# Optimization experiments

Hardware: AMD Instinct MI355X
Metric: run time of the kernel (lower is better)

Reference implementation:

```python
import jax, jax.numpy as jnp
import numpy as np

EPS = 1e-5  # torch LayerNorm default


def _layer_norm(x, g, b):
    mu = jnp.mean(x, axis=-1, keepdims=True)
    var = jnp.mean(jnp.square(x - mu), axis=-1, keepdims=True)
    return (x - mu) * jax.lax.rsqrt(var + EPS) * g + b


def setup_inputs() -> dict:
    key = jax.random.key(0)
    ks = jax.random.split(key, 8)
    B, S, D = 4, 2048, 1024
    s = 1.0 / np.sqrt(D)
    return {
        "q": jax.random.normal(ks[0], (B, S, D), jnp.float32),
        "k": jax.random.normal(ks[1], (B, S, D), jnp.float32),
        "v": jax.random.normal(ks[2], (B, S, D), jnp.float32),
        "mask": jnp.ones((B, 1, S), jnp.int32),
        "Wq": jax.random.normal(ks[3], (D, D), jnp.float32) * s,
        "Wk": jax.random.normal(ks[4], (D, D), jnp.float32) * s,
        "Wv": jax.random.normal(ks[5], (D, D), jnp.float32) * s,
        "Wo": jax.random.normal(ks[6], (D, D), jnp.float32) * s,
        "ln_q_g": jnp.ones((D,), jnp.float32),
        "ln_q_b": jnp.zeros((D,), jnp.float32),
        "ln_k_g": jnp.ones((D,), jnp.float32),
        "ln_k_b": jnp.zeros((D,), jnp.float32),
        "ln_v_g": jnp.ones((D,), jnp.float32),
        "ln_v_b": jnp.zeros((D,), jnp.float32),
    }


def reference(q, k, v, mask, Wq, Wk, Wv, Wo,
              ln_q_g, ln_q_b, ln_k_g, ln_k_b, ln_v_g, ln_v_b):
    B, Lq, D = q.shape
    H = 16
    dk = D // H
    residual = q
    # pre-LN + bias-free projections
    qh = (_layer_norm(q, ln_q_g, ln_q_b) @ Wq).reshape(B, Lq, H, dk).transpose(0, 2, 1, 3)
    kh = (_layer_norm(k, ln_k_g, ln_k_b) @ Wk).reshape(B, -1, H, dk).transpose(0, 2, 1, 3)
    vh = (_layer_norm(v, ln_v_g, ln_v_b) @ Wv).reshape(B, -1, H, dk).transpose(0, 2, 1, 3)
    # scaled scores [B,H,Lq,Lk]
    scores = jnp.einsum('bhqd,bhkd->bhqk', qh, kh) / jnp.sqrt(jnp.float32(dk))
    pad = (mask == 0)[:, None, :, :]  # [B,1,*,Lk], True where masked
    scores = jnp.where(pad, -jnp.inf, scores)
    attn = jax.nn.softmax(scores, axis=-1)
    attn = jnp.where(pad, 0.0, attn)
    out = jnp.einsum('bhqk,bhkd->bhqd', attn, vh)
    out = out.transpose(0, 2, 1, 3).reshape(B, Lq, D)
    return out @ Wo + residual
```

## Files before the change

### kernel.cpp

```cpp
#include <hip/hip_runtime.h>
#include <stdint.h>

typedef __attribute__((ext_vector_type(8))) short short8;
typedef __attribute__((ext_vector_type(4))) float f32x4;
typedef __attribute__((ext_vector_type(4))) unsigned short us4;

#define B_ 4
#define S_ 2048
#define D_ 1024
#define H_ 16
#define DK_ 64

__device__ __forceinline__ unsigned short f2bf(float f) {
  union { float f; unsigned int u; } c; c.f = f;
  unsigned int r = (c.u + 0x7fffu + ((c.u >> 16) & 1u)) >> 16;
  return (unsigned short)r;
}

__device__ __forceinline__ unsigned int cvt_pk_bf16(float lo, float hi) {
  unsigned int r;
  asm("v_cvt_pk_bf16_f32 %0, %1, %2" : "=v"(r) : "v"(lo), "v"(hi));
  return r;
}

__device__ __forceinline__ float exp2_fast(float x) {
#if __has_builtin(__builtin_amdgcn_exp2f)
  return __builtin_amdgcn_exp2f(x);
#else
  float r; asm("v_exp_f32 %0, %1" : "=v"(r) : "v"(x)); return r;
#endif
}

__device__ __forceinline__ void glds16(const void* g, void* l) {
  __builtin_amdgcn_global_load_lds(
      (__attribute__((address_space(1))) void*)(uintptr_t)g,
      (__attribute__((address_space(3))) void*)l, 16, 0, 0);
}

__device__ __forceinline__ f32x4 mfma_bf16(short8 a, short8 b, f32x4 c) {
  return __builtin_amdgcn_mfma_f32_16x16x32_bf16(a, b, c, 0, 0, 0);
}

__global__ __launch_bounds__(256) void ln_bf16_3(const float* __restrict__ x0,
                                                 const float* __restrict__ x1,
                                                 const float* __restrict__ x2,
                                                 const float* __restrict__ g0,
                                                 const float* __restrict__ g1,
                                                 const float* __restrict__ g2,
                                                 const float* __restrict__ b0,
                                                 const float* __restrict__ b1,
                                                 const float* __restrict__ b2,
                                                 unsigned short* __restrict__ y0,
                                                 unsigned short* __restrict__ y1,
                                                 unsigned short* __restrict__ y2) {
  const int which = blockIdx.y;
  const float* x = which == 0 ? x0 : (which == 1 ? x1 : x2);
  const float* g = which == 0 ? g0 : (which == 1 ? g1 : g2);
  const float* bta = which == 0 ? b0 : (which == 1 ? b1 : b2);
  unsigned short* y = which == 0 ? y0 : (which == 1 ? y1 : y2);

  const int lane = threadIdx.x & 63, wid = threadIdx.x >> 6;
  const int row = blockIdx.x * 4 + wid;
  const float4* xr = (const float4*)(x + (size_t)row * D_);
  float4 v[4];
  float s1 = 0.f, s2 = 0.f;
#pragma unroll
  for (int i = 0; i < 4; ++i) {
    v[i] = xr[i * 64 + lane];
    s1 += v[i].x + v[i].y + v[i].z + v[i].w;
    s2 += v[i].x * v[i].x + v[i].y * v[i].y + v[i].z * v[i].z + v[i].w * v[i].w;
  }
#pragma unroll
  for (int m = 32; m; m >>= 1) { s1 += __shfl_xor(s1, m); s2 += __shfl_xor(s2, m); }
  const float mu = s1 * (1.f / D_);
  const float inv = rsqrtf(s2 * (1.f / D_) - mu * mu + 1e-5f);
  const float4* gp = (const float4*)g;
  const float4* bp = (const float4*)bta;
  us4* yr = (us4*)(y + (size_t)row * D_);
#pragma unroll
  for (int i = 0; i < 4; ++i) {
    float4 gv = gp[i * 64 + lane], bv = bp[i * 64 + lane];
    us4 o;
    o[0] = f2bf((v[i].x - mu) * inv * gv.x + bv.x);
    o[1] = f2bf((v[i].y - mu) * inv * gv.y + bv.y);
    o[2] = f2bf((v[i].z - mu) * inv * gv.z + bv.z);
    o[3] = f2bf((v[i].w - mu) * inv * gv.w + bv.w);
    yr[i * 64 + lane] = o;
  }
}

__global__ void wt_bf16_4(const float* __restrict__ W0, const float* __restrict__ W1,
                          const float* __restrict__ W2, const float* __restrict__ W3,
                          unsigned short* __restrict__ T0, unsigned short* __restrict__ T1,
                          unsigned short* __restrict__ T2, unsigned short* __restrict__ T3) {
  const int which = blockIdx.z;
  const float* W = which == 0 ? W0 : (which == 1 ? W1 : (which == 2 ? W2 : W3));
  unsigned short* Wt = which == 0 ? T0 : (which == 1 ? T1 : (which == 2 ? T2 : T3));
  __shared__ float t[32][33];
  const int n0 = blockIdx.x * 32, k0 = blockIdx.y * 32;
  const int tx = threadIdx.x, ty = threadIdx.y;
  for (int i = ty; i < 32; i += 8) t[i][tx] = W[(size_t)(k0 + i) * D_ + n0 + tx];
  __syncthreads();
  for (int i = ty; i < 32; i += 8)
    Wt[(size_t)(n0 + i) * D_ + k0 + tx] = f2bf(t[tx][i]);
}

__global__ __launch_bounds__(256, 2) void gemm_qkv(const unsigned short* __restrict__ Xq,
                                                   const unsigned short* __restrict__ Xk,
                                                   const unsigned short* __restrict__ Xv,
                                                   const unsigned short* __restrict__ Wq,
                                                   const unsigned short* __restrict__ Wk,
                                                   const unsigned short* __restrict__ Wv,
                                                   unsigned short* __restrict__ Qh,
                                                   unsigned short* __restrict__ Kh,
                                                   unsigned short* __restrict__ Vtb,
                                                   float qscale) {
  constexpr int K = D_;
  constexpr int NT = K / 64;
  __shared__ __attribute__((aligned(16))) unsigned short As[2][128][64];
  __shared__ __attribute__((aligned(16))) unsigned short Bs[2][128][64];
  const int z = blockIdx.z;
  const unsigned short* A = z == 0 ? Xq : (z == 1 ? Xk : Xv);
  const unsigned short* Bt = z == 0 ? Wq : (z == 1 ? Wk : Wv);
  const int tid = threadIdx.x;
  const int lane = tid & 63, wid = tid >> 6;
  const int lo16 = lane & 15, hi4 = lane >> 4;
  const int wr = wid >> 1, wc = wid & 1;
  const int gx = (int)gridDim.x;
  const int lid = (int)blockIdx.x + gx * (int)blockIdx.y;
  const int nwg = gx * (int)gridDim.y;
  const int swid = (lid & 7) * (nwg >> 3) + (lid >> 3);
  const int mbase = (swid / gx) * 128, nbase = (swid % gx) * 128;
  const int srow = lane >> 3, scol = (lane & 7) * 8;

  f32x4 acc[4][4] = {};

  auto stage = [&](int bufi, int kt) {
    const int kb = kt * 64;
#pragma unroll
    for (int c = 0; c < 4; ++c) {
      const int ch = wid * 4 + c;
      glds16(A + (size_t)(mbase + ch * 8 + srow) * K + kb + scol,
             (unsigned short*)&As[bufi][0][0] + ch * 512);
      glds16(Bt + (size_t)(nbase + ch * 8 + srow) * K + kb + scol,
             (unsigned short*)&Bs[bufi][0][0] + ch * 512);
    }
  };

  stage(0, 0);
  int cur = 0;

  for (int kt = 0; kt < NT; ++kt) {
    __syncthreads();
    if (kt + 1 < NT) stage(cur ^ 1, kt + 1);
    const unsigned short* Ap = &As[cur][0][0];
    const unsigned short* Bp = &Bs[cur][0][0];
    __builtin_amdgcn_s_setprio(1);
#pragma unroll
    for (int kk = 0; kk < 2; ++kk) {
      short8 af[4], bfr[4];
#pragma unroll
      for (int i = 0; i < 4; ++i)
        af[i] = *(const short8*)(Ap + (wr * 64 + i * 16 + lo16) * 64 + kk * 32 + hi4 * 8);
#pragma unroll
      for (int j = 0; j < 4; ++j)
        bfr[j] = *(const short8*)(Bp + (wc * 64 + j * 16 + lo16) * 64 + kk * 32 + hi4 * 8);
#pragma unroll
      for (int i = 0; i < 4; ++i)
#pragma unroll
        for (int j = 0; j < 4; ++j) acc[i][j] = mfma_bf16(af[i], bfr[j], acc[i][j]);
    }
    __builtin_amdgcn_s_setprio(0);
    cur ^= 1;
  }

  if (z < 2) {
    unsigned short* out = z == 0 ? Qh : Kh;
    const float scale = z == 0 ? qscale : 1.0f;
#pragma unroll
    for (int i = 0; i < 4; ++i) {
      const int row = mbase + wr * 64 + i * 16 + hi4 * 4;
      const int b = row >> 11, s = row & (S_ - 1);
#pragma unroll
      for (int j = 0; j < 4; ++j) {
        const int col = nbase + wc * 64 + j * 16 + lo16;
        const int h = col >> 6, d = col & 63;
        const size_t base = ((size_t)(b * H_ + h) * S_ + s) * DK_ + d;
#pragma unroll
        for (int r = 0; r < 4; ++r) out[base + (size_t)r * DK_] = f2bf(acc[i][j][r] * scale);
      }
    }
  } else {
#pragma unroll
    for (int i = 0; i < 4; ++i) {
      const int row = mbase + wr * 64 + i * 16 + hi4 * 4;
      const int b = row >> 11, s0 = row & (S_ - 1);
#pragma unroll
      for (int j = 0; j < 4; ++j) {
        const int col = nbase + wc * 64 + j * 16 + lo16;
        const int h = col >> 6, d = col & 63;
        us4 w;
#pragma unroll
        for (int r = 0; r < 4; ++r) w[r] = f2bf(acc[i][j][r]);
        *(us4*)(Vtb + ((size_t)(b * H_ + h) * DK_ + d) * S_ + s0) = w;
      }
    }
  }
}

__global__ __launch_bounds__(256, 2) void gemm_out(const unsigned short* __restrict__ A,
                                                   const unsigned short* __restrict__ Bt,
                                                   float* __restrict__ out,
                                                   const float* __restrict__ resid) {
  constexpr int K = D_;
  constexpr int NT = K / 64;
  __shared__ __attribute__((aligned(16))) unsigned short As[2][128][64];
  __shared__ __attribute__((aligned(16))) unsigned short Bs[2][128][64];
  const int tid = threadIdx.x;
  const int lane = tid & 63, wid = tid >> 6;
  const int lo16 = lane & 15, hi4 = lane >> 4;
  const int wr = wid >> 1, wc = wid & 1;
  const int gx = (int)gridDim.x;
  const int lid = (int)blockIdx.x + gx * (int)blockIdx.y;
  const int nwg = gx * (int)gridDim.y;
  const int swid = (lid & 7) * (nwg >> 3) + (lid >> 3);
  const int mbase = (swid / gx) * 128, nbase = (swid % gx) * 128;
  const int srow = lane >> 3, scol = (lane & 7) * 8;

  f32x4 acc[4][4] = {};

  auto stage = [&](int bufi, int kt) {
    const int kb = kt * 64;
#pragma unroll
    for (int c = 0; c < 4; ++c) {
      const int ch = wid * 4 + c;
      glds16(A + (size_t)(mbase + ch * 8 + srow) * K + kb + scol,
             (unsigned short*)&As[bufi][0][0] + ch * 512);
      glds16(Bt + (size_t)(nbase + ch * 8 + srow) * K + kb + scol,
             (unsigned short*)&Bs[bufi][0][0] + ch * 512);
    }
  };

  stage(0, 0);
  int cur = 0;

  for (int kt = 0; kt < NT; ++kt) {
    __syncthreads();
    if (kt + 1 < NT) stage(cur ^ 1, kt + 1);
    const unsigned short* Ap = &As[cur][0][0];
    const unsigned short* Bp = &Bs[cur][0][0];
    __builtin_amdgcn_s_setprio(1);
#pragma unroll
    for (int kk = 0; kk < 2; ++kk) {
      short8 af[4], bfr[4];
#pragma unroll
      for (int i = 0; i < 4; ++i)
        af[i] = *(const short8*)(Ap + (wr * 64 + i * 16 + lo16) * 64 + kk * 32 + hi4 * 8);
#pragma unroll
      for (int j = 0; j < 4; ++j)
        bfr[j] = *(const short8*)(Bp + (wc * 64 + j * 16 + lo16) * 64 + kk * 32 + hi4 * 8);
#pragma unroll
      for (int i = 0; i < 4; ++i)
#pragma unroll
        for (int j = 0; j < 4; ++j) acc[i][j] = mfma_bf16(af[i], bfr[j], acc[i][j]);
    }
    __builtin_amdgcn_s_setprio(0);
    cur ^= 1;
  }

#pragma unroll
  for (int i = 0; i < 4; ++i) {
    const int row = mbase + wr * 64 + i * 16 + hi4 * 4;
#pragma unroll
    for (int j = 0; j < 4; ++j) {
      const int col = nbase + wc * 64 + j * 16 + lo16;
      const size_t idx = (size_t)row * D_ + col;
#pragma unroll
      for (int r = 0; r < 4; ++r)
        out[idx + (size_t)r * D_] = acc[i][j][r] + resid[idx + (size_t)r * D_];
    }
  }
}

__global__ __launch_bounds__(512, 2) void attn_k(const unsigned short* __restrict__ Qh,
                                                 const unsigned short* __restrict__ Kh,
                                                 const unsigned short* __restrict__ Vt,
                                                 const int* __restrict__ mask,
                                                 unsigned short* __restrict__ O) {
  __shared__ __attribute__((aligned(16))) unsigned short Ks[2][64][64];
  __shared__ __attribute__((aligned(16))) unsigned short Vs[2][64][64];
  __shared__ __attribute__((aligned(16))) unsigned short Ps[256][64];
  __shared__ int TileOkI[S_ / 64];
  const int tid = threadIdx.x, lane = tid & 63, wid = tid >> 6;
  const int lo16 = lane & 15, hi4 = lane >> 4;
  const int swz = (lo16 & 7) << 3;
  const int lid = (int)blockIdx.x + 8 * (int)blockIdx.y;
  const int swid = (lid & 7) * 64 + (lid >> 3);
  const int qb = swid & 7, bh = swid >> 3;
  const int b = bh >> 4, h = bh & 15;
  const unsigned short* Qb = Qh + (size_t)bh * S_ * DK_;
  const unsigned short* Kb = Kh + (size_t)bh * S_ * DK_;
  const unsigned short* Vb = Vt + (size_t)bh * DK_ * S_;
  const int* mb = mask + b * S_;
  const int srow = lane >> 3;
  const int scolx = ((lane & 7) ^ srow) * 8;

  if (tid < S_ / 64) TileOkI[tid] = 1;
  __syncthreads();
  {
    int okp = 1;
#pragma unroll
    for (int j = 0; j < 4; ++j) okp &= (mb[tid * 4 + j] != 0);
    if (!okp) TileOkI[tid >> 4] = 0;
  }

  short8 qf[2][2];
#pragma unroll
  for (int i = 0; i < 2; ++i)
#pragma unroll
    for (int kk = 0; kk < 2; ++kk)
      qf[i][kk] = *(const short8*)(Qb + (size_t)(qb * 256 + wid * 32 + i * 16 + lo16) * DK_ +
                                   kk * 32 + hi4 * 8);

  f32x4 o[2][4] = {};
  float lsum0 = 0.f, lsum1 = 0.f;

  auto stageKV = [&](int bufi, int kt) {
    glds16(Kb + (size_t)(kt * 64 + wid * 8 + srow) * DK_ + scolx,
           (unsigned short*)&Ks[bufi][0][0] + wid * 512);
    glds16(Vb + (size_t)(wid * 8 + srow) * S_ + kt * 64 + scolx,
           (unsigned short*)&Vs[bufi][0][0] + wid * 512);
  };

  stageKV(0, 0);
  int cur = 0;

  for (int kt = 0; kt < S_ / 64; ++kt) {
    __syncthreads();
    if (kt + 1 < S_ / 64) stageKV(cur ^ 1, kt + 1);

    const unsigned short* Kc = &Ks[cur][0][0];
    const int tok = TileOkI[kt];
    short8 kf[2][4];
#pragma unroll
    for (int kk = 0; kk < 2; ++kk)
#pragma unroll
      for (int nf = 0; nf < 4; ++nf)
        kf[kk][nf] = *(const short8*)(Kc + (nf * 16 + lo16) * 64 + ((kk * 32 + hi4 * 8) ^ swz));
#pragma unroll
    for (int i = 0; i < 2; ++i) {
      f32x4 p[4] = {};
      __builtin_amdgcn_s_setprio(1);
#pragma unroll
      for (int kk = 0; kk < 2; ++kk)
#pragma unroll
        for (int nf = 0; nf < 4; ++nf) p[nf] = mfma_bf16(kf[kk][nf], qf[i][kk], p[nf]);
      __builtin_amdgcn_s_setprio(0);
      if (!tok) {
#pragma unroll
        for (int nf = 0; nf < 4; ++nf)
#pragma unroll
          for (int r = 0; r < 4; ++r)
            if (mb[kt * 64 + nf * 16 + hi4 * 4 + r] == 0) p[nf][r] = -1e30f;
      }
      const int prow = wid * 32 + i * 16 + lo16;
      float ls = 0.f;
#pragma unroll
      for (int nf = 0; nf < 4; ++nf) {
        float e0 = exp2_fast(p[nf][0]);
        float e1 = exp2_fast(p[nf][1]);
        float e2 = exp2_fast(p[nf][2]);
        float e3 = exp2_fast(p[nf][3]);
        ls += (e0 + e1) + (e2 + e3);
        uint2 w;
        w.x = cvt_pk_bf16(e0, e1);
        w.y = cvt_pk_bf16(e2, e3);
        *(uint2*)&Ps[prow][(nf * 16 + hi4 * 4) ^ swz] = w;
      }
      if (i == 0) lsum0 += ls; else lsum1 += ls;
    }
    asm volatile("s_waitcnt lgkmcnt(0)" ::: "memory");
    __builtin_amdgcn_sched_barrier(0);
    const unsigned short* Vc = &Vs[cur][0][0];
    __builtin_amdgcn_s_setprio(1);
#pragma unroll
    for (int kk = 0; kk < 2; ++kk) {
      const int pc = (kk * 32 + hi4 * 8) ^ swz;
      short8 pa0 = *(const short8*)((const unsigned short*)Ps + (wid * 32 + 0 + lo16) * 64 + pc);
      short8 pa1 = *(const short8*)((const unsigned short*)Ps + (wid * 32 + 16 + lo16) * 64 + pc);
#pragma unroll
      for (int df = 0; df < 4; ++df) {
        short8 vf = *(const short8*)(Vc + (df * 16 + lo16) * 64 + pc);
        o[0][df] = mfma_bf16(pa0, vf, o[0][df]);
        o[1][df] = mfma_bf16(pa1, vf, o[1][df]);
      }
    }
    __builtin_amdgcn_s_setprio(0);
    cur ^= 1;
  }

  lsum0 += __shfl_xor(lsum0, 16); lsum0 += __shfl_xor(lsum0, 32);
  lsum1 += __shfl_xor(lsum1, 16); lsum1 += __shfl_xor(lsum1, 32);
#pragma unroll
  for (int i = 0; i < 2; ++i) {
#pragma unroll
    for (int r = 0; r < 4; ++r) {
      const int ql = hi4 * 4 + r;
      const float l = __shfl(i == 0 ? lsum0 : lsum1, ql);
      const float rl = l > 0.f ? 1.f / l : 0.f;
      const int srowg = qb * 256 + wid * 32 + i * 16 + ql;
      const size_t base = ((size_t)b * S_ + srowg) * D_ + h * 64;
#pragma unroll
      for (int df = 0; df < 4; ++df) O[base + df * 16 + lo16] = f2bf(o[i][df][r] * rl);
    }
  }
}

extern "C" void kernel_launch(void* const* d_in, const int* in_sizes, int n_in,
                              void* d_out, int out_size, void* d_ws, size_t ws_size,
                              hipStream_t stream) {
  const float* q = (const float*)d_in[0];
  const float* k = (const float*)d_in[1];
  const float* v = (const float*)d_in[2];
  const int* mask = (const int*)d_in[3];
  const float* Wq = (const float*)d_in[4];
  const float* Wk = (const float*)d_in[5];
  const float* Wv = (const float*)d_in[6];
  const float* Wo = (const float*)d_in[7];
  const float* lnqg = (const float*)d_in[8];
  const float* lnqb = (const float*)d_in[9];
  const float* lnkg = (const float*)d_in[10];
  const float* lnkb = (const float*)d_in[11];
  const float* lnvg = (const float*)d_in[12];
  const float* lnvb = (const float*)d_in[13];

  uint8_t* ws = (uint8_t*)d_ws;
  const size_t MB = 1024ull * 1024ull;
  unsigned short* Xq = (unsigned short*)(ws + 0 * MB);
  unsigned short* Xk = (unsigned short*)(ws + 16 * MB);
  unsigned short* Xv = (unsigned short*)(ws + 32 * MB);
  unsigned short* Wqt = (unsigned short*)(ws + 48 * MB);
  unsigned short* Wkt = (unsigned short*)(ws + 50 * MB);
  unsigned short* Wvt = (unsigned short*)(ws + 52 * MB);
  unsigned short* Wot = (unsigned short*)(ws + 54 * MB);
  unsigned short* Qh = (unsigned short*)(ws + 56 * MB);
  unsigned short* Kh = (unsigned short*)(ws + 72 * MB);
  unsigned short* Vtb = Xq;
  unsigned short* Ob = Xk;

  hipLaunchKernelGGL(wt_bf16_4, dim3(32, 32, 4), dim3(32, 8), 0, stream,
                     Wq, Wk, Wv, Wo, Wqt, Wkt, Wvt, Wot);

  hipLaunchKernelGGL(ln_bf16_3, dim3(2048, 3), dim3(256), 0, stream,
                     q, k, v, lnqg, lnkg, lnvg, lnqb, lnkb, lnvb, Xq, Xk, Xv);

  const float qscale = 0.125f * 1.4426950408889634f;
  hipLaunchKernelGGL(gemm_qkv, dim3(D_ / 128, (B_ * S_) / 128, 3), dim3(256), 0, stream,
                     Xq, Xk, Xv, Wqt, Wkt, Wvt, Qh, Kh, Vtb, qscale);

  hipLaunchKernelGGL(attn_k, dim3(S_ / 256, B_ * H_), dim3(512), 0, stream, Qh, Kh, Vtb, mask, Ob);

  hipLaunchKernelGGL(gemm_out, dim3(D_ / 128, (B_ * S_) / 128), dim3(256), 0, stream,
                     Ob, Wot, (float*)d_out, q);
}
```

Before: 213.4 us.

## Single-buffer LDS in projection GEMMs and raise occupancy to four blocks

Both projection GEMMs drop their LDS double buffer and use one 32KB stage buffer, loading synchronously with a barrier before and after each k-tile. Launch bounds rise from 2 to 4 blocks per CU. The aim is to hide global-load latency through more resident workgroups instead of intra-block prefetch. In exchange each block loses load/compute overlap, pays an extra barrier per k-tile, and faces a tighter register budget that may cause spills.

```diff
diff --git a/kernel.cpp b/kernel.cpp
--- a/kernel.cpp
+++ b/kernel.cpp
@@ -105,7 +105,7 @@
     Wt[(size_t)(n0 + i) * D_ + k0 + tx] = f2bf(t[tx][i]);
 }
 
-__global__ __launch_bounds__(256, 2) void gemm_qkv(const unsigned short* __restrict__ Xq,
+__global__ __launch_bounds__(256, 4) void gemm_qkv(const unsigned short* __restrict__ Xq,
                                                    const unsigned short* __restrict__ Xk,
                                                    const unsigned short* __restrict__ Xv,
                                                    const unsigned short* __restrict__ Wq,
@@ -117,8 +117,8 @@
                                                    float qscale) {
   constexpr int K = D_;
   constexpr int NT = K / 64;
-  __shared__ __attribute__((aligned(16))) unsigned short As[2][128][64];
-  __shared__ __attribute__((aligned(16))) unsigned short Bs[2][128][64];
+  __shared__ __attribute__((aligned(16))) unsigned short As[128][64];
+  __shared__ __attribute__((aligned(16))) unsigned short Bs[128][64];
   const int z = blockIdx.z;
   const unsigned short* A = z == 0 ? Xq : (z == 1 ? Xk : Xv);
   const unsigned short* Bt = z == 0 ? Wq : (z == 1 ? Wk : Wv);
@@ -135,43 +135,34 @@
 
   f32x4 acc[4][4] = {};
 
-  auto stage = [&](int bufi, int kt) {
+  for (int kt = 0; kt < NT; ++kt) {
+    __syncthreads();
     const int kb = kt * 64;
 #pragma unroll
     for (int c = 0; c < 4; ++c) {
       const int ch = wid * 4 + c;
       glds16(A + (size_t)(mbase + ch * 8 + srow) * K + kb + scol,
-             (unsigned short*)&As[bufi][0][0] + ch * 512);
+             (unsigned short*)As + ch * 512);
       glds16(Bt + (size_t)(nbase + ch * 8 + srow) * K + kb + scol,
-             (unsigned short*)&Bs[bufi][0][0] + ch * 512);
-    }
-  };
-
-  stage(0, 0);
-  int cur = 0;
-
-  for (int kt = 0; kt < NT; ++kt) {
+             (unsigned short*)Bs + ch * 512);
+    }
     __syncthreads();
-    if (kt + 1 < NT) stage(cur ^ 1, kt + 1);
-    const unsigned short* Ap = &As[cur][0][0];
-    const unsigned short* Bp = &Bs[cur][0][0];
     __builtin_amdgcn_s_setprio(1);
 #pragma unroll
     for (int kk = 0; kk < 2; ++kk) {
       short8 af[4], bfr[4];
 #pragma unroll
       for (int i = 0; i < 4; ++i)
-        af[i] = *(const short8*)(Ap + (wr * 64 + i * 16 + lo16) * 64 + kk * 32 + hi4 * 8);
+        af[i] = *(const short8*)(&As[0][0] + (wr * 64 + i * 16 + lo16) * 64 + kk * 32 + hi4 * 8);
 #pragma unroll
       for (int j = 0; j < 4; ++j)
-        bfr[j] = *(const short8*)(Bp + (wc * 64 + j * 16 + lo16) * 64 + kk * 32 + hi4 * 8);
+        bfr[j] = *(const short8*)(&Bs[0][0] + (wc * 64 + j * 16 + lo16) * 64 + kk * 32 + hi4 * 8);
 #pragma unroll
       for (int i = 0; i < 4; ++i)
 #pragma unroll
         for (int j = 0; j < 4; ++j) acc[i][j] = mfma_bf16(af[i], bfr[j], acc[i][j]);
     }
     __builtin_amdgcn_s_setprio(0);
-    cur ^= 1;
   }
 
   if (z < 2) {
@@ -208,14 +199,14 @@
   }
 }
 
-__global__ __launch_bounds__(256, 2) void gemm_out(const unsigned short* __restrict__ A,
+__global__ __launch_bounds__(256, 4) void gemm_out(const unsigned short* __restrict__ A,
                                                    const unsigned short* __restrict__ Bt,
                                                    float* __restrict__ out,
                                                    const float* __restrict__ resid) {
   constexpr int K = D_;
   constexpr int NT = K / 64;
-  __shared__ __attribute__((aligned(16))) unsigned short As[2][128][64];
-  __shared__ __attribute__((aligned(16))) unsigned short Bs[2][128][64];
+  __shared__ __attribute__((aligned(16))) unsigned short As[128][64];
+  __shared__ __attribute__((aligned(16))) unsigned short Bs[128][64];
   const int tid = threadIdx.x;
   const int lane = tid & 63, wid = tid >> 6;
   const int lo16 = lane & 15, hi4 = lane >> 4;
@@ -229,43 +220,34 @@
 
   f32x4 acc[4][4] = {};
 
-  auto stage = [&](int bufi, int kt) {
+  for (int kt = 0; kt < NT; ++kt) {
+    __syncthreads();
     const int kb = kt * 64;
 #pragma unroll
     for (int c = 0; c < 4; ++c) {
       const int ch = wid * 4 + c;
       glds16(A + (size_t)(mbase + ch * 8 + srow) * K + kb + scol,
-             (unsigned short*)&As[bufi][0][0] + ch * 512);
+             (unsigned short*)As + ch * 512);
       glds16(Bt + (size_t)(nbase + ch * 8 + srow) * K + kb + scol,
-             (unsigned short*)&Bs[bufi][0][0] + ch * 512);
-    }
-  };
-
-  stage(0, 0);
-  int cur = 0;
-
-  for (int kt = 0; kt < NT; ++kt) {
+             (unsigned short*)Bs + ch * 512);
+    }
     __syncthreads();
-    if (kt + 1 < NT) stage(cur ^ 1, kt + 1);
-    const unsigned short* Ap = &As[cur][0][0];
-    const unsigned short* Bp = &Bs[cur][0][0];
     __builtin_amdgcn_s_setprio(1);
 #pragma unroll
     for (int kk = 0; kk < 2; ++kk) {
       short8 af[4], bfr[4];
 #pragma unroll
       for (int i = 0; i < 4; ++i)
-        af[i] = *(const short8*)(Ap + (wr * 64 + i * 16 + lo16) * 64 + kk * 32 + hi4 * 8);
+        af[i] = *(const short8*)(&As[0][0] + (wr * 64 + i * 16 + lo16) * 64 + kk * 32 + hi4 * 8);
 #pragma unroll
       for (int j = 0; j < 4; ++j)
-        bfr[j] = *(const short8*)(Bp + (wc * 64 + j * 16 + lo16) * 64 + kk * 32 + hi4 * 8);
+        bfr[j] = *(const short8*)(&Bs[0][0] + (wc * 64 + j * 16 + lo16) * 64 + kk * 32 + hi4 * 8);
 #pragma unroll
       for (int i = 0; i < 4; ++i)
 #pragma unroll
         for (int j = 0; j < 4; ++j) acc[i][j] = mfma_bf16(af[i], bfr[j], acc[i][j]);
     }
     __builtin_amdgcn_s_setprio(0);
-    cur ^= 1;
   }
 
 #pragma unroll
```

After: 202.2 us (median of 2 runs). 1.06x faster.
